# Kernel tuning notes

Hardware: AMD Instinct MI355X
Metric: run time of the kernel (lower is better)

Reference implementation:

```python
import jax, jax.numpy as jnp
import numpy as np

N, T, D, N_BINS = 2048, 256, 64, 64
REG = 1.0


def _batched_histogram(x, a, b, n_bins):
    """Replicates torch.histc(x[:, t, i], bins=n_bins, min=a[t,i], max=b[t,i]) / N
    for every (t, i) pair in one fused scatter.
    x: [N, T, D]; a, b: [T, D]. Returns normalized counts [T, D, n_bins]."""
    T_, D_ = a.shape
    width = b - a  # [T, D]
    # bin index; values exactly at the right edge fall into the last bin (torch.histc behavior)
    idx = jnp.clip(jnp.floor((x - a[None]) / width[None] * n_bins), 0, n_bins - 1).astype(jnp.int32)
    # torch.histc ignores values outside [min, max]
    in_range = ((x >= a[None]) & (x <= b[None])).astype(x.dtype)
    base = (jnp.arange(T_, dtype=jnp.int32)[:, None] * D_
            + jnp.arange(D_, dtype=jnp.int32)[None, :]) * n_bins  # [T, D]
    flat_idx = (base[None] + idx).reshape(-1)  # [N*T*D]
    counts = jax.ops.segment_sum(in_range.reshape(-1), flat_idx,
                                 num_segments=T_ * D_ * n_bins)
    # normalize=True in histogram_torch: divide by num elements (= N, since x_ti is [N,1])
    return counts.reshape(T_, D_, n_bins) / x.shape[0]


def setup_inputs() -> dict:
    key = jax.random.key(0)
    k_real, k_fake = jax.random.split(key)
    x_real = jax.random.normal(k_real, (N, T, D), dtype=jnp.float32)
    x_fake = jax.random.normal(k_fake, (N, T, D), dtype=jnp.float32) * 1.1 + 0.05
    # __init__ precomputation: per-(t,i) min/max and normalized real histogram
    bin_min = x_real.min(axis=0)  # [T, D]
    bin_max = x_real.max(axis=0)
    bin_max = jnp.where(bin_max == bin_min, bin_max + 1e-05, bin_max)
    densities = _batched_histogram(x_real, bin_min, bin_max, N_BINS)  # [T, D, n_bins]
    return {"x_fake": x_fake, "densities": densities,
            "bin_min": bin_min, "bin_max": bin_max}


def reference(x_fake, densities, bin_min, bin_max):
    n_bins = densities.shape[-1]
    d_fake = _batched_histogram(x_fake, bin_min, bin_max, n_bins)  # [T, D, n_bins]
    # per-(i,t) mean over bins of |d_fake - d_real|, stacked then averaged,
    # which equals a global mean over [T, D, n_bins]
    loss_componentwise_mean = jnp.mean(jnp.abs(d_fake - densities))
    return REG * loss_componentwise_mean
```

## Files before the change

kernel.cpp:

```cpp
#include <hip/hip_runtime.h>

constexpr int N_SAMP = 2048;
constexpr int T_DIM  = 256;
constexpr int D_DIM  = 64;
constexpr int NBINS  = 64;

__global__ __launch_bounds__(1024) void histo_loss_kernel(
    const float* __restrict__ x,
    const float* __restrict__ dens,
    const float* __restrict__ bmin,
    const float* __restrict__ bmax,
    float* __restrict__ partial)
{
    __shared__ unsigned int hist[D_DIM * NBINS];
    const int t   = blockIdx.x;
    const int tid = threadIdx.x;

    for (int i = tid; i < D_DIM * NBINS; i += 1024) hist[i] = 0u;

    const int c  = tid & 15;
    const int r  = tid >> 4;
    const int d0 = c * 4;

    const float4 a4 = *reinterpret_cast<const float4*>(bmin + t * D_DIM + d0);
    const float4 b4 = *reinterpret_cast<const float4*>(bmax + t * D_DIM + d0);
    const float a[4] = {a4.x, a4.y, a4.z, a4.w};
    const float b[4] = {b4.x, b4.y, b4.z, b4.w};
    float s[4];
#pragma unroll
    for (int j = 0; j < 4; ++j) s[j] = (float)NBINS / (b[j] - a[j]);

    __syncthreads();

    const float4* __restrict__ x4 = reinterpret_cast<const float4*>(x);
    const size_t row4 = (size_t)(T_DIM * D_DIM / 4);
    const size_t base = (size_t)r * row4 + (size_t)t * (D_DIM / 4) + (size_t)c;

#pragma unroll 4
    for (int it = 0; it < N_SAMP / 64; ++it) {
        float4 v4 = x4[base + (size_t)it * 64 * row4];
        float v[4] = {v4.x, v4.y, v4.z, v4.w};
#pragma unroll
        for (int j = 0; j < 4; ++j) {
            float vv = v[j];
            if (vv >= a[j] && vv <= b[j]) {
                int idx = (int)floorf((vv - a[j]) * s[j]);
                idx = idx < 0 ? 0 : (idx > NBINS - 1 ? NBINS - 1 : idx);
                atomicAdd(&hist[(d0 + j) * NBINS + idx], 1u);
            }
        }
    }
    __syncthreads();

    const float invN = 1.0f / (float)N_SAMP;
    const float* __restrict__ db = dens + (size_t)t * (D_DIM * NBINS);
    float sum = 0.0f;
#pragma unroll
    for (int k = 0; k < (D_DIM * NBINS) / 1024; ++k) {
        int f = k * 1024 + tid;
        sum += fabsf((float)hist[f] * invN - db[f]);
    }
#pragma unroll
    for (int off = 32; off > 0; off >>= 1) sum += __shfl_down(sum, off, 64);

    __shared__ float wpart[16];
    if ((tid & 63) == 0) wpart[tid >> 6] = sum;
    __syncthreads();
    if (tid < 16) {
        float v = wpart[tid];
#pragma unroll
        for (int off = 8; off > 0; off >>= 1) v += __shfl_down(v, off, 16);
        if (tid == 0) partial[t] = v;
    }
}

__global__ __launch_bounds__(256) void histo_final_reduce(
    const float* __restrict__ partial, float* __restrict__ out)
{
    const int tid = threadIdx.x;
    float v = partial[tid];
#pragma unroll
    for (int off = 32; off > 0; off >>= 1) v += __shfl_down(v, off, 64);
    __shared__ float wpart[4];
    if ((tid & 63) == 0) wpart[tid >> 6] = v;
    __syncthreads();
    if (tid == 0) {
        float tot = (wpart[0] + wpart[1]) + (wpart[2] + wpart[3]);
        out[0] = tot * (1.0f / (float)(T_DIM * D_DIM * NBINS));
    }
}

extern "C" void kernel_launch(void* const* d_in, const int* in_sizes, int n_in,
                              void* d_out, int out_size, void* d_ws, size_t ws_size,
                              hipStream_t stream)
{
    const float* x    = (const float*)d_in[0];
    const float* dens = (const float*)d_in[1];
    const float* bmin = (const float*)d_in[2];
    const float* bmax = (const float*)d_in[3];
    float* out     = (float*)d_out;
    float* partial = (float*)d_ws;

    histo_loss_kernel<<<T_DIM, 1024, 0, stream>>>(x, dens, bmin, bmax, partial);
    histo_final_reduce<<<1, 256, 0, stream>>>(partial, out);
}
```

Before: 27.17 us.

## Fuse final reduction into histogram kernel via last-block atomic counter

Replaces the separate final-reduce launch with a last-block-done pattern: each block publishes its partial sum with release semantics and bumps an atomic counter, and the last block reduces all partials and writes the output. A memset of the counter is added to the stream, so a small launch remains. The bin-index computation drops floorf and the lower clamp, relying on in-range values being non-negative offsets, and the density comparison uses vectorized float4/uint4 loads.

```diff
diff --git a/kernel.cpp b/kernel.cpp
--- a/kernel.cpp
+++ b/kernel.cpp
@@ -5,14 +5,16 @@
 constexpr int D_DIM  = 64;
 constexpr int NBINS  = 64;
 
-__global__ __launch_bounds__(1024) void histo_loss_kernel(
+__global__ __launch_bounds__(1024) void histo_loss_fused(
     const float* __restrict__ x,
     const float* __restrict__ dens,
     const float* __restrict__ bmin,
     const float* __restrict__ bmax,
-    float* __restrict__ partial)
+    float* __restrict__ partial,
+    unsigned int* __restrict__ counter,
+    float* __restrict__ out)
 {
-    __shared__ unsigned int hist[D_DIM * NBINS];
+    __shared__ alignas(16) unsigned int hist[D_DIM * NBINS];
     const int t   = blockIdx.x;
     const int tid = threadIdx.x;
 
@@ -44,8 +46,8 @@
         for (int j = 0; j < 4; ++j) {
             float vv = v[j];
             if (vv >= a[j] && vv <= b[j]) {
-                int idx = (int)floorf((vv - a[j]) * s[j]);
-                idx = idx < 0 ? 0 : (idx > NBINS - 1 ? NBINS - 1 : idx);
+                int idx = (int)((vv - a[j]) * s[j]);
+                idx = idx > NBINS - 1 ? NBINS - 1 : idx;
                 atomicAdd(&hist[(d0 + j) * NBINS + idx], 1u);
             }
         }
@@ -54,39 +56,47 @@
 
     const float invN = 1.0f / (float)N_SAMP;
     const float* __restrict__ db = dens + (size_t)t * (D_DIM * NBINS);
-    float sum = 0.0f;
-#pragma unroll
-    for (int k = 0; k < (D_DIM * NBINS) / 1024; ++k) {
-        int f = k * 1024 + tid;
-        sum += fabsf((float)hist[f] * invN - db[f]);
-    }
+    const int f = tid * 4;
+    float4 dv = *reinterpret_cast<const float4*>(db + f);
+    uint4  hv = *reinterpret_cast<const uint4*>(hist + f);
+    float sum = fabsf((float)hv.x * invN - dv.x)
+              + fabsf((float)hv.y * invN - dv.y)
+              + fabsf((float)hv.z * invN - dv.z)
+              + fabsf((float)hv.w * invN - dv.w);
 #pragma unroll
     for (int off = 32; off > 0; off >>= 1) sum += __shfl_down(sum, off, 64);
 
     __shared__ float wpart[16];
     if ((tid & 63) == 0) wpart[tid >> 6] = sum;
     __syncthreads();
-    if (tid < 16) {
-        float v = wpart[tid];
+
+    __shared__ bool isLast;
+    if (tid == 0) {
+        float v = 0.0f;
 #pragma unroll
-        for (int off = 8; off > 0; off >>= 1) v += __shfl_down(v, off, 16);
-        if (tid == 0) partial[t] = v;
+        for (int w = 0; w < 16; ++w) v += wpart[w];
+        __hip_atomic_store(&partial[t], v, __ATOMIC_RELEASE, __HIP_MEMORY_SCOPE_AGENT);
+        unsigned int prev = __hip_atomic_fetch_add(counter, 1u, __ATOMIC_ACQ_REL,
+                                                   __HIP_MEMORY_SCOPE_AGENT);
+        isLast = (prev == (unsigned int)(T_DIM - 1));
     }
-}
+    __syncthreads();
 
-__global__ __launch_bounds__(256) void histo_final_reduce(
-    const float* __restrict__ partial, float* __restrict__ out)
-{
-    const int tid = threadIdx.x;
-    float v = partial[tid];
+    if (isLast) {
+        float v = 0.0f;
+        if (tid < T_DIM)
+            v = __hip_atomic_load(&partial[tid], __ATOMIC_ACQUIRE, __HIP_MEMORY_SCOPE_AGENT);
 #pragma unroll
-    for (int off = 32; off > 0; off >>= 1) v += __shfl_down(v, off, 64);
-    __shared__ float wpart[4];
-    if ((tid & 63) == 0) wpart[tid >> 6] = v;
-    __syncthreads();
-    if (tid == 0) {
-        float tot = (wpart[0] + wpart[1]) + (wpart[2] + wpart[3]);
-        out[0] = tot * (1.0f / (float)(T_DIM * D_DIM * NBINS));
+        for (int off = 32; off > 0; off >>= 1) v += __shfl_down(v, off, 64);
+        __shared__ float wpart2[16];
+        if ((tid & 63) == 0) wpart2[tid >> 6] = v;
+        __syncthreads();
+        if (tid == 0) {
+            float tot = 0.0f;
+#pragma unroll
+            for (int w = 0; w < 16; ++w) tot += wpart2[w];
+            out[0] = tot * (1.0f / (float)(T_DIM * D_DIM * NBINS));
+        }
     }
 }
 
@@ -100,7 +110,9 @@
     const float* bmax = (const float*)d_in[3];
     float* out     = (float*)d_out;
     float* partial = (float*)d_ws;
+    unsigned int* counter = (unsigned int*)((char*)d_ws + 1024);
 
-    histo_loss_kernel<<<T_DIM, 1024, 0, stream>>>(x, dens, bmin, bmax, partial);
-    histo_final_reduce<<<1, 256, 0, stream>>>(partial, out);
+    hipMemsetAsync(counter, 0, sizeof(unsigned int), stream);
+    histo_loss_fused<<<T_DIM, 1024, 0, stream>>>(x, dens, bmin, bmax,
+                                                 partial, counter, out);
 }
```

Measured after the change: 37.71 us. 38.8% more time.
